# Kernel optimization log

Measured on AMD Instinct MI355X. Metric: run time of the kernel, lower is better.

The kernel has to match this reference:

```python
import jax, jax.numpy as jnp
import numpy as np

D = 192   # token_dim == channel_dim == expert_dim == adapt_dim (required by source code)
S = 4096  # sequence length
NE = 8    # num_experts


def _ln(x, g, b, eps=1e-5):
    m = x.mean(-1, keepdims=True)
    v = ((x - m) ** 2).mean(-1, keepdims=True)
    return (x - m) / jnp.sqrt(v + eps) * g + b


def _adaptive(x, a, W, b, AW, Ab):
    # AdaptiveLinear with adapt_method='add': weight = W + adapt(a).view(out, in)
    dW = (AW @ a + Ab).reshape(W.shape)
    return x @ (W + dW).T + b


def setup_inputs() -> dict:
    key = jax.random.key(0)
    ks = iter(jax.random.split(key, 40))

    def n(shape, s=0.05):
        return jax.random.normal(next(ks), shape, dtype=jnp.float32) * s

    return {
        "x": n((1, S, D), 1.0),
        "W_in": n((D, D)), "b_in": n((D,)),
        "feat_W": n((D, D)), "feat_b": n((D,)),
        "feat_AW": n((D * D, D)), "feat_Ab": n((D * D,)),
        "an_g": jnp.ones((D,)), "an_b": jnp.zeros((D,)),
        "tm_W": n((D, D)), "tm_b": n((D,)),
        "tm_AW": n((D * D, D)), "tm_Ab": n((D * D,)),
        "tn_g": jnp.ones((D,)), "tn_b": jnp.zeros((D,)),
        "cm_W": n((D, D)), "cm_b": n((D,)),
        "cm_AW": n((D * D, D)), "cm_Ab": n((D * D,)),
        "cn_g": jnp.ones((D,)), "cn_b": jnp.zeros((D,)),
        "pm_W": n((D, D)), "pm_b": n((D,)),
        "gate_W": n((NE, D)), "gate_b": n((NE,)),
        "ex_W": n((NE, D, D)), "ex_b": n((NE, D)),
        "ex_AW": n((NE, D * D, D)), "ex_Ab": n((NE, D * D)),
        "mn_g": jnp.ones((D,)), "mn_b": jnp.zeros((D,)),
        "out_W": n((D, D)), "out_b": n((D,)),
    }


def reference(x, W_in, b_in, feat_W, feat_b, feat_AW, feat_Ab, an_g, an_b,
              tm_W, tm_b, tm_AW, tm_Ab, tn_g, tn_b,
              cm_W, cm_b, cm_AW, cm_Ab, cn_g, cn_b,
              pm_W, pm_b, gate_W, gate_b, ex_W, ex_b, ex_AW, ex_Ab,
              mn_g, mn_b, out_W, out_b):
    h = x @ W_in.T + b_in                                        # [1,S,D]
    xm = h.mean(axis=1)                                          # [1,D]
    a = _adaptive(xm, xm[0], feat_W, feat_b, feat_AW, feat_Ab)   # [1,D]
    a = _ln(a, an_g, an_b)
    a0 = a[0]                                                    # [D]
    t = _adaptive(h, a0, tm_W, tm_b, tm_AW, tm_Ab)               # token mixing
    t = _ln(t, tn_g, tn_b)
    c = _adaptive(t, a0, cm_W, cm_b, cm_AW, cm_Ab)               # channel mixing
    c = _ln(c, cn_g, cn_b)
    m = c @ pm_W.T + pm_b                                        # pre-MoE [1,S,D]
    gate = jax.nn.softmax(a @ gate_W.T + gate_b, axis=-1)[0]     # [NE]
    # batched hypernet weight generation for all experts at once
    dW = (jnp.einsum('eka,a->ek', ex_AW, a0) + ex_Ab).reshape(NE, D, D)
    We = ex_W + dW                                               # [NE,D,D]
    ye = jnp.einsum('bsd,ned->nbse', m, We) + ex_b[:, None, None, :]
    eo = jnp.einsum('n,nbse->bse', gate, ye)                     # soft-MoE sum
    eo = _ln(eo, mn_g, mn_b)
    eo = jax.nn.relu(eo)
    return eo @ out_W.T + out_b
```

## Files before the change

### kernel.cpp

```cpp
#include <hip/hip_runtime.h>

#define DD 192

template <int EMIT, int LNL>
__global__ __launch_bounds__(256) void stage3_k(
    const float* __restrict__ A, const float* __restrict__ W,
    const float* __restrict__ bias,
    const float* __restrict__ stats_in, const float* __restrict__ lng,
    const float* __restrict__ lnb,
    float* __restrict__ out, float* __restrict__ emit_buf) {
    __shared__ float At[32 * 200];
    __shared__ float WT[DD * 64];
    __shared__ float ms[32], rs[32];
    __shared__ float csum[4 * 64];

    const int t = threadIdx.x;
    const int tr = t >> 5, tc = t & 31;
    const int b = blockIdx.x;
    const int cg = b % 3;
    const int c0 = cg * 64;
    const int r0 = (b / 3) * 32;

    if (LNL > 0) {
        if (t < 32) {
            int r = r0 + t;
            float s = stats_in[2 * r] + stats_in[8192 + 2 * r] + stats_in[16384 + 2 * r];
            float q = stats_in[2 * r + 1] + stats_in[8192 + 2 * r + 1]
                    + stats_in[16384 + 2 * r + 1];
            float mean = s * (1.f / 192.f);
            float var = q * (1.f / 192.f) - mean * mean;
            ms[t] = mean;
            rs[t] = rsqrtf(var + 1e-5f);
        }
        __syncthreads();
    }

    {
        const float4* A4 = (const float4*)(A + (size_t)r0 * DD);
#pragma unroll
        for (int q = 0; q < 6; q++) {
            int f = t + 256 * q;
            int r = f / 48, jj = f - r * 48;
            float4 v = A4[f];
            if (LNL > 0) {
                float mean = ms[r], rstd = rs[r];
                float4 g4 = ((const float4*)lng)[jj];
                float4 b4 = ((const float4*)lnb)[jj];
                v.x = (v.x - mean) * rstd * g4.x + b4.x;
                v.y = (v.y - mean) * rstd * g4.y + b4.y;
                v.z = (v.z - mean) * rstd * g4.z + b4.z;
                v.w = (v.w - mean) * rstd * g4.w + b4.w;
                if (LNL == 2) {
                    v.x = fmaxf(v.x, 0.f); v.y = fmaxf(v.y, 0.f);
                    v.z = fmaxf(v.z, 0.f); v.w = fmaxf(v.w, 0.f);
                }
            }
            *(float4*)&At[r * 200 + 4 * jj] = v;
        }
    }
    {
        const float4* W4 = (const float4*)(W + (size_t)c0 * DD);
#pragma unroll
        for (int q = 0; q < 12; q++) {
            int f = t + 256 * q;
            int ip = f / 48, jj = f - ip * 48;
            float4 v = W4[f];
            int j0 = 4 * jj;
            WT[(j0 + 0) * 64 + ((ip + 2 * ((j0 + 0) & 31)) & 63)] = v.x;
            WT[(j0 + 1) * 64 + ((ip + 2 * ((j0 + 1) & 31)) & 63)] = v.y;
            WT[(j0 + 2) * 64 + ((ip + 2 * ((j0 + 2) & 31)) & 63)] = v.z;
            WT[(j0 + 3) * 64 + ((ip + 2 * ((j0 + 3) & 31)) & 63)] = v.w;
        }
    }

    const int i0 = c0 + 2 * tc;
    float bv0 = bias[i0], bv1 = bias[i0 + 1];
    float acc[4][2];
#pragma unroll
    for (int i = 0; i < 4; i++) { acc[i][0] = bv0; acc[i][1] = bv1; }
    __syncthreads();

    const int rbase = 4 * tr;
#pragma unroll 2
    for (int jc = 0; jc < DD; jc += 8) {
        float a_[4][8];
#pragma unroll
        for (int rr = 0; rr < 4; rr++) {
            float4 u = *(const float4*)&At[(rbase + rr) * 200 + jc];
            float4 v = *(const float4*)&At[(rbase + rr) * 200 + jc + 4];
            a_[rr][0] = u.x; a_[rr][1] = u.y; a_[rr][2] = u.z; a_[rr][3] = u.w;
            a_[rr][4] = v.x; a_[rr][5] = v.y; a_[rr][6] = v.z; a_[rr][7] = v.w;
        }
#pragma unroll
        for (int jj = 0; jj < 8; jj++) {
            const int j = jc + jj;
            int cs = (2 * tc + 2 * (j & 31)) & 63;
            float2 w2 = *(const float2*)&WT[j * 64 + cs];
            acc[0][0] = fmaf(a_[0][jj], w2.x, acc[0][0]);
            acc[0][1] = fmaf(a_[0][jj], w2.y, acc[0][1]);
            acc[1][0] = fmaf(a_[1][jj], w2.x, acc[1][0]);
            acc[1][1] = fmaf(a_[1][jj], w2.y, acc[1][1]);
            acc[2][0] = fmaf(a_[2][jj], w2.x, acc[2][0]);
            acc[2][1] = fmaf(a_[2][jj], w2.y, acc[2][1]);
            acc[3][0] = fmaf(a_[3][jj], w2.x, acc[3][0]);
            acc[3][1] = fmaf(a_[3][jj], w2.y, acc[3][1]);
        }
    }

#pragma unroll
    for (int i = 0; i < 4; i++) {
        int row = r0 + rbase + i;
        *(float2*)&out[(size_t)row * DD + i0] = make_float2(acc[i][0], acc[i][1]);
    }

    if (EMIT == 2) {
#pragma unroll
        for (int i = 0; i < 4; i++) {
            float s = acc[i][0] + acc[i][1];
            float q = acc[i][0] * acc[i][0] + acc[i][1] * acc[i][1];
#pragma unroll
            for (int m = 16; m >= 1; m >>= 1) {
                s += __shfl_xor(s, m);
                q += __shfl_xor(q, m);
            }
            if (tc == 0) {
                int r = r0 + rbase + i;
                emit_buf[cg * 8192 + 2 * r] = s;
                emit_buf[cg * 8192 + 2 * r + 1] = q;
            }
        }
    } else if (EMIT == 1) {
        float cs0 = acc[0][0] + acc[1][0] + acc[2][0] + acc[3][0];
        float cs1 = acc[0][1] + acc[1][1] + acc[2][1] + acc[3][1];
        cs0 += __shfl_xor(cs0, 32);
        cs1 += __shfl_xor(cs1, 32);
        int w = t >> 6;
        if ((t & 63) < 32) {
            csum[w * 64 + 2 * tc] = cs0;
            csum[w * 64 + 2 * tc + 1] = cs1;
        }
        __syncthreads();
        if (t < 64) {
            float s = csum[t] + csum[64 + t] + csum[128 + t] + csum[192 + t];
            atomicAdd(&emit_buf[c0 + t], s);
        }
    }
}

__global__ __launch_bounds__(256) void hyper_k(
    const float* __restrict__ tm_W, const float* __restrict__ tm_AW,
    const float* __restrict__ tm_Ab, const float* __restrict__ cm_W,
    const float* __restrict__ cm_AW, const float* __restrict__ cm_Ab,
    const float* __restrict__ ex_W, const float* __restrict__ ex_AW,
    const float* __restrict__ ex_Ab, const float* __restrict__ a0g,
    const float* __restrict__ gateg, float* __restrict__ Wt,
    float* __restrict__ Wc, float* __restrict__ Wmoe) {
    __shared__ float a0s[DD];
    __shared__ float rows[32 * 204];
    __shared__ float wb[32], ab[32], vals[32];
    __shared__ float gs[8];
    const int t = threadIdx.x;
    const int b = blockIdx.x;
    const int r = t >> 3, p = t & 7;
    if (t < DD) a0s[t] = a0g[t];

    if (b < 2304) {
        const float* AW; const float* WB; const float* AB; float* dst;
        int k0;
        if (b < 1152) { AW = tm_AW; WB = tm_W; AB = tm_Ab; dst = Wt; k0 = b * 32; }
        else          { AW = cm_AW; WB = cm_W; AB = cm_Ab; dst = Wc; k0 = (b - 1152) * 32; }
        if (t < 32) { wb[t] = WB[k0 + t]; ab[t] = AB[k0 + t]; }
        const float4* src4 = (const float4*)(AW + (size_t)k0 * DD);
#pragma unroll
        for (int q = 0; q < 6; q++) {
            int fidx = t + 256 * q;
            int rr = fidx / 48, jj = fidx - rr * 48;
            *(float4*)&rows[rr * 204 + 4 * jj] = src4[fidx];
        }
        __syncthreads();
        float acc = 0.f;
#pragma unroll
        for (int q = 0; q < 6; q++) {
            int jo = p * 24 + 4 * q;
            float4 w = *(const float4*)&rows[r * 204 + jo];
            float4 aa = *(const float4*)&a0s[jo];
            acc = fmaf(w.x, aa.x, acc); acc = fmaf(w.y, aa.y, acc);
            acc = fmaf(w.z, aa.z, acc); acc = fmaf(w.w, aa.w, acc);
        }
        acc += __shfl_xor(acc, 1);
        acc += __shfl_xor(acc, 2);
        acc += __shfl_xor(acc, 4);
        if (p == 0) vals[r] = acc + wb[r] + ab[r];
        __syncthreads();
        if (t < 32) dst[k0 + t] = vals[t];
    } else {
        const int k0 = (b - 2304) * 32;
        if (t < 8) gs[t] = gateg[t];
        float macc = 0.f;
        for (int e = 0; e < 8; e++) {
            __syncthreads();
            const float4* src4 =
                (const float4*)(ex_AW + (size_t)e * 36864 * DD + (size_t)k0 * DD);
#pragma unroll
            for (int q = 0; q < 6; q++) {
                int fidx = t + 256 * q;
                int rr = fidx / 48, jj = fidx - rr * 48;
                *(float4*)&rows[rr * 204 + 4 * jj] = src4[fidx];
            }
            __syncthreads();
            float acc = 0.f;
#pragma unroll
            for (int q = 0; q < 6; q++) {
                int jo = p * 24 + 4 * q;
                float4 w = *(const float4*)&rows[r * 204 + jo];
                float4 aa = *(const float4*)&a0s[jo];
                acc = fmaf(w.x, aa.x, acc); acc = fmaf(w.y, aa.y, acc);
                acc = fmaf(w.z, aa.z, acc); acc = fmaf(w.w, aa.w, acc);
            }
            acc += __shfl_xor(acc, 1);
            acc += __shfl_xor(acc, 2);
            acc += __shfl_xor(acc, 4);
            if (p == 0) vals[r] = acc;
            __syncthreads();
            if (t < 32) {
                float we = ex_W[(size_t)e * 36864 + k0 + t];
                float ae = ex_Ab[(size_t)e * 36864 + k0 + t];
                macc = fmaf(gs[e], vals[t] + we + ae, macc);
            }
        }
        if (t < 32) Wmoe[k0 + t] = macc;
    }
}

__global__ __launch_bounds__(256) void feat2_k(
    const float* __restrict__ feat_W, const float* __restrict__ feat_AW,
    const float* __restrict__ feat_Ab, const float* __restrict__ xm_sum,
    float* __restrict__ a_pre) {
    __shared__ float xms[DD];
    __shared__ float rows[32 * 204];
    __shared__ float wb[32], ab[32], vals[32];
    const int t = threadIdx.x;
    const int k0 = blockIdx.x * 32;
    if (t < DD) xms[t] = xm_sum[t] * (1.f / 4096.f);
    if (t < 32) { wb[t] = feat_W[k0 + t]; ab[t] = feat_Ab[k0 + t]; }
    const float4* src4 = (const float4*)(feat_AW + (size_t)k0 * DD);
#pragma unroll
    for (int q = 0; q < 6; q++) {
        int fidx = t + 256 * q;
        int r = fidx / 48, jj = fidx - r * 48;
        float4 v = src4[fidx];
        *(float4*)&rows[r * 204 + 4 * jj] = v;
    }
    __syncthreads();
    const int r = t >> 3, p = t & 7;
    float acc = 0.f;
#pragma unroll
    for (int q = 0; q < 6; q++) {
        int jo = p * 24 + 4 * q;
        float4 w = *(const float4*)&rows[r * 204 + jo];
        float4 aa = *(const float4*)&xms[jo];
        acc = fmaf(w.x, aa.x, acc); acc = fmaf(w.y, aa.y, acc);
        acc = fmaf(w.z, aa.z, acc); acc = fmaf(w.w, aa.w, acc);
    }
    acc += __shfl_xor(acc, 1);
    acc += __shfl_xor(acc, 2);
    acc += __shfl_xor(acc, 4);
    if (p == 0) vals[r] = acc + wb[r] + ab[r];
    __syncthreads();
    const int j0 = k0 % DD;
    if (t < 32) {
        float c = vals[t] * xms[j0 + t];
#pragma unroll
        for (int m = 16; m >= 1; m >>= 1) c += __shfl_xor(c, m);
        if (t == 0) atomicAdd(&a_pre[k0 / DD], c);
    }
}

__global__ __launch_bounds__(192) void vec_k(
    const float* __restrict__ a_pre, const float* __restrict__ feat_b,
    const float* __restrict__ an_g, const float* __restrict__ an_b,
    const float* __restrict__ gate_W, const float* __restrict__ gate_b,
    const float* __restrict__ ex_b, float* __restrict__ a0g,
    float* __restrict__ gateg, float* __restrict__ b_moe) {
    __shared__ float red[6];
    __shared__ float gred[24];
    __shared__ float lgs[8];
    const int t = threadIdx.x;
    const int w = t >> 6;
    float v = a_pre[t] + feat_b[t];
    float s = v, q = v * v;
#pragma unroll
    for (int m = 32; m >= 1; m >>= 1) {
        s += __shfl_xor(s, m);
        q += __shfl_xor(q, m);
    }
    if ((t & 63) == 0) { red[w] = s; red[3 + w] = q; }
    __syncthreads();
    float S = red[0] + red[1] + red[2];
    float Q = red[3] + red[4] + red[5];
    float mean = S * (1.f / 192.f);
    float var = Q * (1.f / 192.f) - mean * mean;
    float rstd = rsqrtf(var + 1e-5f);
    float a0v = (v - mean) * rstd * an_g[t] + an_b[t];
    a0g[t] = a0v;
#pragma unroll
    for (int e = 0; e < 8; e++) {
        float x = a0v * gate_W[e * DD + t];
#pragma unroll
        for (int m = 32; m >= 1; m >>= 1) x += __shfl_xor(x, m);
        if ((t & 63) == 0) gred[w * 8 + e] = x;
    }
    __syncthreads();
    if (t < 8) lgs[t] = gred[t] + gred[8 + t] + gred[16 + t] + gate_b[t];
    __syncthreads();
    if (t == 0) {
        float mx = lgs[0];
        for (int e = 1; e < 8; e++) mx = fmaxf(mx, lgs[e]);
        float sum = 0.f, ex[8];
        for (int e = 0; e < 8; e++) { ex[e] = expf(lgs[e] - mx); sum += ex[e]; }
        for (int e = 0; e < 8; e++) lgs[e] = ex[e] / sum;
    }
    __syncthreads();
    if (t < 8) gateg[t] = lgs[t];
    float bm = 0.f;
#pragma unroll
    for (int e = 0; e < 8; e++) bm = fmaf(lgs[e], ex_b[e * DD + t], bm);
    b_moe[t] = bm;
}

extern "C" void kernel_launch(void* const* d_in, const int* in_sizes, int n_in,
                              void* d_out, int out_size, void* d_ws, size_t ws_size,
                              hipStream_t stream) {
    (void)in_sizes; (void)n_in; (void)out_size; (void)ws_size;
    const float* x       = (const float*)d_in[0];
    const float* W_in    = (const float*)d_in[1];
    const float* b_in    = (const float*)d_in[2];
    const float* feat_W  = (const float*)d_in[3];
    const float* feat_b  = (const float*)d_in[4];
    const float* feat_AW = (const float*)d_in[5];
    const float* feat_Ab = (const float*)d_in[6];
    const float* an_g    = (const float*)d_in[7];
    const float* an_b    = (const float*)d_in[8];
    const float* tm_W    = (const float*)d_in[9];
    const float* tm_b    = (const float*)d_in[10];
    const float* tm_AW   = (const float*)d_in[11];
    const float* tm_Ab   = (const float*)d_in[12];
    const float* tn_g    = (const float*)d_in[13];
    const float* tn_b    = (const float*)d_in[14];
    const float* cm_W    = (const float*)d_in[15];
    const float* cm_b    = (const float*)d_in[16];
    const float* cm_AW   = (const float*)d_in[17];
    const float* cm_Ab   = (const float*)d_in[18];
    const float* cn_g    = (const float*)d_in[19];
    const float* cn_b    = (const float*)d_in[20];
    const float* pm_W    = (const float*)d_in[21];
    const float* pm_b    = (const float*)d_in[22];
    const float* gate_W  = (const float*)d_in[23];
    const float* gate_b  = (const float*)d_in[24];
    const float* ex_W    = (const float*)d_in[25];
    const float* ex_b    = (const float*)d_in[26];
    const float* ex_AW   = (const float*)d_in[27];
    const float* ex_Ab   = (const float*)d_in[28];
    const float* mn_g    = (const float*)d_in[29];
    const float* mn_b    = (const float*)d_in[30];
    const float* out_W   = (const float*)d_in[31];
    const float* out_b   = (const float*)d_in[32];

    float* ws = (float*)d_ws;
    float* B0     = ws;
    float* B1     = ws + 786432;
    float* xm_sum = ws + 1572864;
    float* a_pre  = ws + 1573056;
    float* Wmoe   = ws + 1573248;
    float* Wt     = ws + 1610112;
    float* Wc     = ws + 1646976;
    float* st1    = ws + 1683840;
    float* st2    = ws + 1708416;
    float* st3    = ws + 1732992;
    float* a0     = ws + 1757568;
    float* gate   = ws + 1757760;
    float* b_moe  = ws + 1757768;

    hipMemsetAsync(xm_sum, 0, (size_t)384 * sizeof(float), stream);

    stage3_k<1, 0><<<384, 256, 0, stream>>>(x, W_in, b_in, nullptr, nullptr, nullptr,
                                            B0, xm_sum);
    feat2_k<<<1152, 256, 0, stream>>>(feat_W, feat_AW, feat_Ab, xm_sum, a_pre);
    vec_k<<<1, 192, 0, stream>>>(a_pre, feat_b, an_g, an_b, gate_W, gate_b, ex_b,
                                 a0, gate, b_moe);
    hyper_k<<<3456, 256, 0, stream>>>(tm_W, tm_AW, tm_Ab, cm_W, cm_AW, cm_Ab,
                                      ex_W, ex_AW, ex_Ab, a0, gate, Wt, Wc, Wmoe);
    stage3_k<2, 0><<<384, 256, 0, stream>>>(B0, Wt, tm_b, nullptr, nullptr, nullptr,
                                            B1, st1);
    stage3_k<2, 1><<<384, 256, 0, stream>>>(B1, Wc, cm_b, st1, tn_g, tn_b, B0, st2);
    stage3_k<0, 1><<<384, 256, 0, stream>>>(B0, pm_W, pm_b, st2, cn_g, cn_b, B1, nullptr);
    stage3_k<2, 0><<<384, 256, 0, stream>>>(B1, Wmoe, b_moe, nullptr, nullptr, nullptr,
                                            B0, st3);
    stage3_k<0, 2><<<384, 256, 0, stream>>>(B0, out_W, out_b, st3, mn_g, mn_b,
                                            (float*)d_out, nullptr);
}
```

Measured before the change: 532.5 us.

## Stream hypernet weights directly from global memory and drop atomics in mean reduction

The hypernetwork GEMV kernels stop staging AW rows through shared memory. Each 8-thread group now reads its row straight from global memory and keeps the adapt vector in registers. The expert path prefetches the next expert's row while computing the current one. The column-sum for the sequence mean now writes per-block partials instead of using atomics, which removes the memset. feat2_k now runs 192 blocks, each reducing a full output element, which avoids atomics but gives fewer blocks to stream feat_AW.

```diff
diff --git a/kernel.cpp b/kernel.cpp
--- a/kernel.cpp
+++ b/kernel.cpp
@@ -142,138 +142,55 @@
         __syncthreads();
         if (t < 64) {
             float s = csum[t] + csum[64 + t] + csum[128 + t] + csum[192 + t];
-            atomicAdd(&emit_buf[c0 + t], s);
-        }
-    }
-}
-
-__global__ __launch_bounds__(256) void hyper_k(
-    const float* __restrict__ tm_W, const float* __restrict__ tm_AW,
-    const float* __restrict__ tm_Ab, const float* __restrict__ cm_W,
-    const float* __restrict__ cm_AW, const float* __restrict__ cm_Ab,
-    const float* __restrict__ ex_W, const float* __restrict__ ex_AW,
-    const float* __restrict__ ex_Ab, const float* __restrict__ a0g,
-    const float* __restrict__ gateg, float* __restrict__ Wt,
-    float* __restrict__ Wc, float* __restrict__ Wmoe) {
-    __shared__ float a0s[DD];
-    __shared__ float rows[32 * 204];
-    __shared__ float wb[32], ab[32], vals[32];
-    __shared__ float gs[8];
+            emit_buf[(size_t)(b / 3) * DD + c0 + t] = s;
+        }
+    }
+}
+
+__global__ __launch_bounds__(256) void feat2_k(
+    const float* __restrict__ feat_W, const float* __restrict__ feat_AW,
+    const float* __restrict__ feat_Ab, const float* __restrict__ part,
+    float* __restrict__ a_pre) {
+    __shared__ float xms[DD];
+    __shared__ float wsum[4];
     const int t = threadIdx.x;
-    const int b = blockIdx.x;
-    const int r = t >> 3, p = t & 7;
-    if (t < DD) a0s[t] = a0g[t];
-
-    if (b < 2304) {
-        const float* AW; const float* WB; const float* AB; float* dst;
-        int k0;
-        if (b < 1152) { AW = tm_AW; WB = tm_W; AB = tm_Ab; dst = Wt; k0 = b * 32; }
-        else          { AW = cm_AW; WB = cm_W; AB = cm_Ab; dst = Wc; k0 = (b - 1152) * 32; }
-        if (t < 32) { wb[t] = WB[k0 + t]; ab[t] = AB[k0 + t]; }
-        const float4* src4 = (const float4*)(AW + (size_t)k0 * DD);
+    const int i = blockIdx.x;
+    if (t < DD) {
+        float s = 0.f;
+        for (int rg = 0; rg < 128; rg++) s += part[rg * DD + t];
+        xms[t] = s * (1.f / 4096.f);
+    }
+    __syncthreads();
+    const int p = t & 7, rsub = t >> 3;
+    float xsl[24];
+#pragma unroll
+    for (int q = 0; q < 6; q++) {
+        float4 v = *(const float4*)&xms[p * 4 + 32 * q];
+        xsl[4*q] = v.x; xsl[4*q+1] = v.y; xsl[4*q+2] = v.z; xsl[4*q+3] = v.w;
+    }
+    float bacc = 0.f;
+    for (int pass = 0; pass < 6; pass++) {
+        int j = pass * 32 + rsub;
+        size_t k = (size_t)i * DD + j;
+        const float4* row4 = (const float4*)(feat_AW + k * DD);
+        float acc = 0.f;
 #pragma unroll
         for (int q = 0; q < 6; q++) {
-            int fidx = t + 256 * q;
-            int rr = fidx / 48, jj = fidx - rr * 48;
-            *(float4*)&rows[rr * 204 + 4 * jj] = src4[fidx];
-        }
-        __syncthreads();
-        float acc = 0.f;
-#pragma unroll
-        for (int q = 0; q < 6; q++) {
-            int jo = p * 24 + 4 * q;
-            float4 w = *(const float4*)&rows[r * 204 + jo];
-            float4 aa = *(const float4*)&a0s[jo];
-            acc = fmaf(w.x, aa.x, acc); acc = fmaf(w.y, aa.y, acc);
-            acc = fmaf(w.z, aa.z, acc); acc = fmaf(w.w, aa.w, acc);
+            float4 w = row4[p + 8 * q];
+            acc = fmaf(w.x, xsl[4*q], acc);   acc = fmaf(w.y, xsl[4*q+1], acc);
+            acc = fmaf(w.z, xsl[4*q+2], acc); acc = fmaf(w.w, xsl[4*q+3], acc);
         }
         acc += __shfl_xor(acc, 1);
         acc += __shfl_xor(acc, 2);
         acc += __shfl_xor(acc, 4);
-        if (p == 0) vals[r] = acc + wb[r] + ab[r];
-        __syncthreads();
-        if (t < 32) dst[k0 + t] = vals[t];
-    } else {
-        const int k0 = (b - 2304) * 32;
-        if (t < 8) gs[t] = gateg[t];
-        float macc = 0.f;
-        for (int e = 0; e < 8; e++) {
-            __syncthreads();
-            const float4* src4 =
-                (const float4*)(ex_AW + (size_t)e * 36864 * DD + (size_t)k0 * DD);
-#pragma unroll
-            for (int q = 0; q < 6; q++) {
-                int fidx = t + 256 * q;
-                int rr = fidx / 48, jj = fidx - rr * 48;
-                *(float4*)&rows[rr * 204 + 4 * jj] = src4[fidx];
-            }
-            __syncthreads();
-            float acc = 0.f;
-#pragma unroll
-            for (int q = 0; q < 6; q++) {
-                int jo = p * 24 + 4 * q;
-                float4 w = *(const float4*)&rows[r * 204 + jo];
-                float4 aa = *(const float4*)&a0s[jo];
-                acc = fmaf(w.x, aa.x, acc); acc = fmaf(w.y, aa.y, acc);
-                acc = fmaf(w.z, aa.z, acc); acc = fmaf(w.w, aa.w, acc);
-            }
-            acc += __shfl_xor(acc, 1);
-            acc += __shfl_xor(acc, 2);
-            acc += __shfl_xor(acc, 4);
-            if (p == 0) vals[r] = acc;
-            __syncthreads();
-            if (t < 32) {
-                float we = ex_W[(size_t)e * 36864 + k0 + t];
-                float ae = ex_Ab[(size_t)e * 36864 + k0 + t];
-                macc = fmaf(gs[e], vals[t] + we + ae, macc);
-            }
-        }
-        if (t < 32) Wmoe[k0 + t] = macc;
-    }
-}
-
-__global__ __launch_bounds__(256) void feat2_k(
-    const float* __restrict__ feat_W, const float* __restrict__ feat_AW,
-    const float* __restrict__ feat_Ab, const float* __restrict__ xm_sum,
-    float* __restrict__ a_pre) {
-    __shared__ float xms[DD];
-    __shared__ float rows[32 * 204];
-    __shared__ float wb[32], ab[32], vals[32];
-    const int t = threadIdx.x;
-    const int k0 = blockIdx.x * 32;
-    if (t < DD) xms[t] = xm_sum[t] * (1.f / 4096.f);
-    if (t < 32) { wb[t] = feat_W[k0 + t]; ab[t] = feat_Ab[k0 + t]; }
-    const float4* src4 = (const float4*)(feat_AW + (size_t)k0 * DD);
-#pragma unroll
-    for (int q = 0; q < 6; q++) {
-        int fidx = t + 256 * q;
-        int r = fidx / 48, jj = fidx - r * 48;
-        float4 v = src4[fidx];
-        *(float4*)&rows[r * 204 + 4 * jj] = v;
-    }
-    __syncthreads();
-    const int r = t >> 3, p = t & 7;
-    float acc = 0.f;
-#pragma unroll
-    for (int q = 0; q < 6; q++) {
-        int jo = p * 24 + 4 * q;
-        float4 w = *(const float4*)&rows[r * 204 + jo];
-        float4 aa = *(const float4*)&xms[jo];
-        acc = fmaf(w.x, aa.x, acc); acc = fmaf(w.y, aa.y, acc);
-        acc = fmaf(w.z, aa.z, acc); acc = fmaf(w.w, aa.w, acc);
-    }
-    acc += __shfl_xor(acc, 1);
-    acc += __shfl_xor(acc, 2);
-    acc += __shfl_xor(acc, 4);
-    if (p == 0) vals[r] = acc + wb[r] + ab[r];
-    __syncthreads();
-    const int j0 = k0 % DD;
-    if (t < 32) {
-        float c = vals[t] * xms[j0 + t];
-#pragma unroll
-        for (int m = 16; m >= 1; m >>= 1) c += __shfl_xor(c, m);
-        if (t == 0) atomicAdd(&a_pre[k0 / DD], c);
-    }
+        if (p == 0) bacc = fmaf(acc + feat_W[k] + feat_Ab[k], xms[j], bacc);
+    }
+    bacc += __shfl_xor(bacc, 8);
+    bacc += __shfl_xor(bacc, 16);
+    bacc += __shfl_xor(bacc, 32);
+    if ((t & 63) == 0) wsum[t >> 6] = bacc;
+    __syncthreads();
+    if (t == 0) a_pre[i] = wsum[0] + wsum[1] + wsum[2] + wsum[3];
 }
 
 __global__ __launch_bounds__(192) void vec_k(
@@ -290,10 +207,7 @@
     float v = a_pre[t] + feat_b[t];
     float s = v, q = v * v;
 #pragma unroll
-    for (int m = 32; m >= 1; m >>= 1) {
-        s += __shfl_xor(s, m);
-        q += __shfl_xor(q, m);
-    }
+    for (int m = 32; m >= 1; m >>= 1) { s += __shfl_xor(s, m); q += __shfl_xor(q, m); }
     if ((t & 63) == 0) { red[w] = s; red[3 + w] = q; }
     __syncthreads();
     float S = red[0] + red[1] + red[2];
@@ -326,6 +240,82 @@
 #pragma unroll
     for (int e = 0; e < 8; e++) bm = fmaf(lgs[e], ex_b[e * DD + t], bm);
     b_moe[t] = bm;
+}
+
+__global__ __launch_bounds__(256) void hyper_k(
+    const float* __restrict__ tm_W, const float* __restrict__ tm_AW,
+    const float* __restrict__ tm_Ab, const float* __restrict__ cm_W,
+    const float* __restrict__ cm_AW, const float* __restrict__ cm_Ab,
+    const float* __restrict__ ex_W, const float* __restrict__ ex_AW,
+    const float* __restrict__ ex_Ab, const float* __restrict__ a0g,
+    const float* __restrict__ gateg, float* __restrict__ Wt,
+    float* __restrict__ Wc, float* __restrict__ Wmoe) {
+    const int t = threadIdx.x, b = blockIdx.x;
+    const int p = t & 7, rsub = t >> 3;
+    float asl[24];
+#pragma unroll
+    for (int q = 0; q < 6; q++) {
+        float4 v = *(const float4*)&a0g[p * 4 + 32 * q];
+        asl[4*q] = v.x; asl[4*q+1] = v.y; asl[4*q+2] = v.z; asl[4*q+3] = v.w;
+    }
+    if (b < 1152) {
+        const int kk = b * 32 + rsub;
+        float gv[8];
+#pragma unroll
+        for (int e = 0; e < 8; e++) gv[e] = gateg[e];
+        float4 wv[6], wn[6];
+        {
+            const float4* row4 = (const float4*)(ex_AW + (size_t)kk * DD);
+#pragma unroll
+            for (int q = 0; q < 6; q++) wv[q] = row4[p + 8 * q];
+        }
+        float macc = 0.f;
+#pragma unroll
+        for (int e = 0; e < 8; e++) {
+            if (e < 7) {
+                const float4* nr =
+                    (const float4*)(ex_AW + ((size_t)(e + 1) * 36864 + kk) * DD);
+#pragma unroll
+                for (int q = 0; q < 6; q++) wn[q] = nr[p + 8 * q];
+            }
+            float acc = 0.f;
+#pragma unroll
+            for (int q = 0; q < 6; q++) {
+                acc = fmaf(wv[q].x, asl[4*q], acc);
+                acc = fmaf(wv[q].y, asl[4*q+1], acc);
+                acc = fmaf(wv[q].z, asl[4*q+2], acc);
+                acc = fmaf(wv[q].w, asl[4*q+3], acc);
+            }
+            acc += __shfl_xor(acc, 1);
+            acc += __shfl_xor(acc, 2);
+            acc += __shfl_xor(acc, 4);
+            macc = fmaf(gv[e],
+                        acc + ex_W[(size_t)e * 36864 + kk] + ex_Ab[(size_t)e * 36864 + kk],
+                        macc);
+#pragma unroll
+            for (int q = 0; q < 6; q++) wv[q] = wn[q];
+        }
+        if (p == 0) Wmoe[kk] = macc;
+    } else {
+        const bool isT = b < 2304;
+        const int kk = (isT ? b - 1152 : b - 2304) * 32 + rsub;
+        const float* AW = isT ? tm_AW : cm_AW;
+        const float* WB = isT ? tm_W : cm_W;
+        const float* AB = isT ? tm_Ab : cm_Ab;
+        float* dst = isT ? Wt : Wc;
+        const float4* row4 = (const float4*)(AW + (size_t)kk * DD);
+        float acc = 0.f;
+#pragma unroll
+        for (int q = 0; q < 6; q++) {
+            float4 w = row4[p + 8 * q];
+            acc = fmaf(w.x, asl[4*q], acc);   acc = fmaf(w.y, asl[4*q+1], acc);
+            acc = fmaf(w.z, asl[4*q+2], acc); acc = fmaf(w.w, asl[4*q+3], acc);
+        }
+        acc += __shfl_xor(acc, 1);
+        acc += __shfl_xor(acc, 2);
+        acc += __shfl_xor(acc, 4);
+        if (p == 0) dst[kk] = acc + WB[kk] + AB[kk];
+    }
 }
 
 extern "C" void kernel_launch(void* const* d_in, const int* in_sizes, int n_in,
@@ -369,23 +359,22 @@
     float* ws = (float*)d_ws;
     float* B0     = ws;
     float* B1     = ws + 786432;
-    float* xm_sum = ws + 1572864;
-    float* a_pre  = ws + 1573056;
-    float* Wmoe   = ws + 1573248;
-    float* Wt     = ws + 1610112;
-    float* Wc     = ws + 1646976;
-    float* st1    = ws + 1683840;
-    float* st2    = ws + 1708416;
-    float* st3    = ws + 1732992;
-    float* a0     = ws + 1757568;
-    float* gate   = ws + 1757760;
-    float* b_moe  = ws + 1757768;
-
-    hipMemsetAsync(xm_sum, 0, (size_t)384 * sizeof(float), stream);
+    float* part   = ws + 1572864;
+    float* Wmoe   = ws + 1597440;
+    float* Wt     = ws + 1634304;
+    float* Wc     = ws + 1671168;
+    float* st1    = ws + 1708032;
+    float* st2    = ws + 1732608;
+    float* st3    = ws + 1757184;
+    float* a_pre  = ws + 1781760;
+    float* a0     = ws + 1781952;
+    float* gate   = ws + 1782144;
+    float* b_moe  = ws + 1782152;
+
 
     stage3_k<1, 0><<<384, 256, 0, stream>>>(x, W_in, b_in, nullptr, nullptr, nullptr,
-                                            B0, xm_sum);
-    feat2_k<<<1152, 256, 0, stream>>>(feat_W, feat_AW, feat_Ab, xm_sum, a_pre);
+                                            B0, part);
+    feat2_k<<<192, 256, 0, stream>>>(feat_W, feat_AW, feat_Ab, part, a_pre);
     vec_k<<<1, 192, 0, stream>>>(a_pre, feat_b, an_g, an_b, gate_W, gate_b, ex_b,
                                  a0, gate, b_moe);
     hyper_k<<<3456, 256, 0, stream>>>(tm_W, tm_AW, tm_Ab, cm_W, cm_AW, cm_Ab,
```

New measurement: 538.3 us. Within noise of the previous version (+1.1%).
